# Kernel optimization log

Hardware: AMD Instinct MI355X
Metric: run time of the kernel (lower is better)

Reference implementation:

```python
import jax, jax.numpy as jnp
import numpy as np

IN_CH = 512
HEADS = 8
DIM_HEAD = 64
HIDDEN = HEADS * DIM_HEAD


def rms_norm(x, g):
    # torch F.normalize(x, dim=1): x / max(||x||_2 along channel, eps)
    norm = jnp.sqrt(jnp.sum(x * x, axis=1, keepdims=True))
    xn = x / jnp.maximum(norm, 1e-12)
    return xn * g * (x.shape[1] ** 0.5)


def setup_inputs() -> dict:
    key = jax.random.key(0)
    ks = jax.random.split(key, 6)
    x = jax.random.normal(ks[0], (8, IN_CH, 8192), dtype=jnp.float32)
    g1 = jnp.ones((1, IN_CH, 1), dtype=jnp.float32)
    # Conv1d k=1 weights stored as [out, in]
    w_qkv = jax.random.normal(ks[1], (3 * HIDDEN, IN_CH), dtype=jnp.float32) * (IN_CH ** -0.5)
    w_out = jax.random.normal(ks[2], (IN_CH, HIDDEN), dtype=jnp.float32) * (HIDDEN ** -0.5)
    b_out = jax.random.normal(ks[3], (IN_CH,), dtype=jnp.float32) * 0.01
    g2 = jnp.ones((1, IN_CH, 1), dtype=jnp.float32)
    return {"x": x, "g1": g1, "w_qkv": w_qkv, "w_out": w_out, "b_out": b_out, "g2": g2}


def reference(x, g1, w_qkv, w_out, b_out, g2):
    b, c, l = x.shape
    h, dh = HEADS, DIM_HEAD
    scale = dh ** -0.5
    xn = rms_norm(x, g1)
    # 1x1 conv == channel matmul: [b,3*hidden,l]
    qkv = jnp.einsum('oc,bcl->bol', w_qkv, xn)
    q, k, v = jnp.split(qkv, 3, axis=1)
    q = q.reshape(b, h, dh, l)
    k = k.reshape(b, h, dh, l)
    v = v.reshape(b, h, dh, l)
    q = jax.nn.softmax(q, axis=2) * scale  # softmax over head-dim channels
    k = jax.nn.softmax(k, axis=3)          # softmax over sequence
    context = jnp.einsum('bhdn,bhen->bhde', k, v)  # [b,h,dh,dh]
    out = jnp.einsum('bhde,bhdn->bhen', context, q)
    out = out.reshape(b, h * dh, l)
    out = jnp.einsum('oc,bcl->bol', w_out, out) + b_out[None, :, None]
    return rms_norm(out, g2)
```

## Files before the change

### kernel.cpp

```cpp
#include <hip/hip_runtime.h>
#include <hip/hip_bf16.h>


typedef short short8 __attribute__((ext_vector_type(8)));
typedef short short4v __attribute__((ext_vector_type(4)));
typedef float f32x4 __attribute__((ext_vector_type(4)));
typedef unsigned short ushort;

#define SQRT512 22.627416997969522f

__device__ __forceinline__ ushort f2bf(float f){
  union{float f; unsigned u;} v; v.f = f;
  unsigned r = v.u + 0x7fffu + ((v.u >> 16) & 1u);
  return (ushort)(r >> 16);
}

__device__ __forceinline__ void gload16(const void* g, void* l){
  __builtin_amdgcn_global_load_lds(
      (const __attribute__((address_space(1))) unsigned int*)(unsigned long long)g,
      (__attribute__((address_space(3))) unsigned int*)(unsigned int)(unsigned long long)l,
      16, 0, 0);
}

__global__ void k_prep_w1(const float* __restrict__ wqkv, const float* __restrict__ g1,
                          ushort* __restrict__ W1){
  int i = blockIdx.x * 256 + threadIdx.x;
  int c = i & 511;
  W1[i] = f2bf(wqkv[i] * g1[c] * SQRT512);
}

__global__ __launch_bounds__(256) void k_xt(const float* __restrict__ x,
                                            ushort* __restrict__ Xt,
                                            float* __restrict__ invnorm){
  __shared__ __align__(16) ushort tile[64*132];
  __shared__ float ssq[4][64];
  int b = blockIdx.y, lb = blockIdx.x;
  int t = threadIdx.x, lane = t & 63, crow = t >> 6;
  const float* xb = x + ((size_t)b*512)*8192 + (size_t)lb*64;
  float acc = 0.f;
  for(int c0 = 0; c0 < 512; c0 += 128){
    __syncthreads();
    for(int cc = crow; cc < 128; cc += 4){
      float v = xb[(size_t)(c0+cc)*8192 + lane];
      acc += v*v;
      tile[lane*132 + cc] = f2bf(v);
    }
    __syncthreads();
    ushort* dst = Xt + ((size_t)(b*8192 + lb*64))*512 + c0;
    int ch = t & 31;
    for(int r = t >> 5; r < 64; r += 8){
      short4v vv = *(const short4v*)&tile[r*132 + ch*4];
      *(short4v*)(dst + (size_t)r*512 + ch*4) = vv;
    }
  }
  ssq[crow][lane] = acc;
  __syncthreads();
  if(t < 64){
    float s = ssq[0][t] + ssq[1][t] + ssq[2][t] + ssq[3][t];
    invnorm[b*8192 + lb*64 + t] = 1.f / fmaxf(sqrtf(s), 1e-12f);
  }
}

__global__ __launch_bounds__(512,4) void k_qkv(
    const ushort* __restrict__ W1, const ushort* __restrict__ Xt,
    const float* __restrict__ invnorm,
    ushort* __restrict__ Qt, float* __restrict__ ctxp, float* __restrict__ kpart){
  __shared__ __align__(16) union U {
    ushort buf[2][12288];
    struct { ushort P[8192]; ushort Vb[8192]; } e;
  } S;
  __shared__ float ksum[128];

  int bid = blockIdx.x;
  int wg  = (bid & 7)*384 + (bid >> 3);
  int b   = wg / 384;
  int rem = wg % 384;
  int grp = rem / 12, s = rem % 12;
  bool isQ = (s < 4);
  int t = threadIdx.x, lane = t & 63, w = t >> 6;
  int rsub = lane >> 2;
  int pc   = (lane & 3) ^ ((lane >> 3) & 3);

  int r = 0, ct2 = 0, hb = 0, ct = 0;
  const ushort* Aq = W1;
  const ushort* Bbase;
  if(isQ){ r = s; ct2 = grp;
    Aq = W1 + (size_t)(r*128)*512;
    Bbase = Xt + ((size_t)(b*8192 + ct2*256))*512;
  } else { int t2 = s - 4; ct = 2*grp + (t2 & 1); hb = t2 >> 1;
    Bbase = Xt + ((size_t)(b*8192 + ct*128))*512;
  }
  if(t < 128) ksum[t] = 0.f;

  f32x4 acc[4][4] = {};

  auto stage = [&](int ks, int cb){
    int goff = ks*32 + pc*8;
    if(isQ){
      ushort* A  = S.buf[cb];
      ushort* Bl = S.buf[cb] + 4096;
      gload16(Aq    + (size_t)(w*16 + rsub)*512 + goff, A + w*512);
      gload16(Bbase + (size_t)(w*32 + rsub)*512 + goff, Bl + w*1024);
      gload16(Bbase + (size_t)(w*32 + 16 + rsub)*512 + goff, Bl + w*1024 + 512);
    } else {
      ushort* A  = S.buf[cb];
      ushort* Bl = S.buf[cb] + 8192;
      int lr0 = w*32 + rsub;
      int gr0 = (w < 4) ? (512 + hb*128 + lr0) : (1024 + hb*128 + (lr0 - 128));
      gload16(W1 + (size_t)gr0*512 + goff, A + w*1024);
      gload16(W1 + (size_t)(gr0 + 16)*512 + goff, A + w*1024 + 512);
      gload16(Bbase + (size_t)(w*16 + rsub)*512 + goff, Bl + w*512);
    }
  };

  auto compute = [&](int cb){
    const ushort *A, *Bl; int aw, bw;
    if(isQ){ A = S.buf[cb]; Bl = S.buf[cb] + 4096; aw = w >> 2; bw = w & 3; }
    else   { A = S.buf[cb]; Bl = S.buf[cb] + 8192; aw = w >> 1; bw = w & 1; }
    int g = lane >> 4;
    short8 af[4], bf[4];
#pragma unroll
    for(int m4 = 0; m4 < 4; ++m4){ int ra = aw*64 + m4*16 + (lane & 15);
      af[m4] = *(const short8*)&A[ra*32 + (g ^ ((ra >> 1) & 3))*8]; }
#pragma unroll
    for(int n4 = 0; n4 < 4; ++n4){ int rb = bw*64 + n4*16 + (lane & 15);
      bf[n4] = *(const short8*)&Bl[rb*32 + (g ^ ((rb >> 1) & 3))*8]; }
#pragma unroll
    for(int m4 = 0; m4 < 4; ++m4)
#pragma unroll
      for(int n4 = 0; n4 < 4; ++n4)
        acc[m4][n4] = __builtin_amdgcn_mfma_f32_16x16x32_bf16(af[m4], bf[n4], acc[m4][n4], 0,0,0);
  };

  stage(0, 0);
#pragma unroll
  for(int ks = 0; ks < 16; ++ks){
    int cur = ks & 1;
    if(ks < 15){ stage(ks + 1, cur ^ 1);
                 asm volatile("s_waitcnt vmcnt(3)" ::: "memory"); }
    else       { asm volatile("s_waitcnt vmcnt(0)" ::: "memory"); }
    __builtin_amdgcn_s_barrier();
    compute(cur);
    asm volatile("s_waitcnt lgkmcnt(0)" ::: "memory");
    __builtin_amdgcn_s_barrier();
  }

  if(isQ){
    int wr = w >> 2, wc = w & 3;
    float cs[4];
    const float* invb = invnorm + b*8192 + ct2*256;
#pragma unroll
    for(int n4 = 0; n4 < 4; ++n4) cs[n4] = invb[wc*64 + n4*16 + (lane & 15)];
    float mx[4] = {-3e38f,-3e38f,-3e38f,-3e38f};
#pragma unroll
    for(int m4 = 0; m4 < 4; ++m4)
#pragma unroll
      for(int n4 = 0; n4 < 4; ++n4)
#pragma unroll
        for(int j = 0; j < 4; ++j){
          float v = acc[m4][n4][j]*cs[n4];
          acc[m4][n4][j] = v;
          mx[n4] = fmaxf(mx[n4], v);
        }
#pragma unroll
    for(int n4 = 0; n4 < 4; ++n4){
      mx[n4] = fmaxf(mx[n4], __shfl_xor(mx[n4], 16));
      mx[n4] = fmaxf(mx[n4], __shfl_xor(mx[n4], 32));
    }
    float sm[4] = {0.f,0.f,0.f,0.f};
#pragma unroll
    for(int m4 = 0; m4 < 4; ++m4)
#pragma unroll
      for(int n4 = 0; n4 < 4; ++n4)
#pragma unroll
        for(int j = 0; j < 4; ++j){
          float e = __expf(acc[m4][n4][j] - mx[n4]);
          acc[m4][n4][j] = e;
          sm[n4] += e;
        }
    float inv[4];
#pragma unroll
    for(int n4 = 0; n4 < 4; ++n4){
      sm[n4] += __shfl_xor(sm[n4], 16);
      sm[n4] += __shfl_xor(sm[n4], 32);
      inv[n4] = 0.125f / sm[n4];
    }
#pragma unroll
    for(int n4 = 0; n4 < 4; ++n4){
      int col = ct2*256 + wc*64 + n4*16 + (lane & 15);
      ushort* dst = Qt + ((size_t)(b*8192 + col))*512 + r*128 + wr*64 + (lane >> 4)*4;
#pragma unroll
      for(int m4 = 0; m4 < 4; ++m4){
        short4v p;
#pragma unroll
        for(int j = 0; j < 4; ++j) p[j] = (short)f2bf(acc[m4][n4][j]*inv[n4]);
        *(short4v*)(dst + m4*16) = p;
      }
    }
  } else {
    int wr2 = w >> 1, bw = w & 1;
    bool isK = (w < 4);
    float cs[4];
    const float* invb = invnorm + b*8192 + ct*128;
#pragma unroll
    for(int n4 = 0; n4 < 4; ++n4) cs[n4] = invb[bw*64 + n4*16 + (lane & 15)];
    int hq = w >> 2, rq = w & 3;
    f32x4 c2[4] = {};
#pragma unroll
    for(int hl = 0; hl < 2; ++hl){
      __syncthreads();
      if(bw == hl){
#pragma unroll
        for(int m4 = 0; m4 < 4; ++m4)
#pragma unroll
          for(int j = 0; j < 4; ++j){
            int row = wr2*64 + m4*16 + (lane >> 4)*4 + j;
            float rs = 0.f;
#pragma unroll
            for(int n4 = 0; n4 < 4; ++n4){
              int lc = n4*16 + (lane & 15);
              float val = acc[m4][n4][j]*cs[n4];
              if(isK){
                float e = __expf(val); rs += e;
                S.e.P[row*64 + ((lc >> 3) ^ (row & 7))*8 + (lc & 7)] = f2bf(e);
              } else {
                int er = row - 128;
                S.e.Vb[er*64 + ((lc >> 3) ^ (er & 7))*8 + (lc & 7)] = f2bf(val);
              }
            }
            if(isK) atomicAdd(&ksum[row], rs);
          }
      }
      __syncthreads();
#pragma unroll
      for(int kk = 0; kk < 2; ++kk){
        int g2 = kk*4 + (lane >> 4);
        int da = hq*64 + rq*16 + (lane & 15);
        short8 pa = *(const short8*)&S.e.P[da*64 + (g2 ^ (da & 7))*8];
#pragma unroll
        for(int n4 = 0; n4 < 4; ++n4){
          int eb = hq*64 + n4*16 + (lane & 15);
          short8 vb = *(const short8*)&S.e.Vb[eb*64 + (g2 ^ (eb & 7))*8];
          c2[n4] = __builtin_amdgcn_mfma_f32_16x16x32_bf16(pa, vb, c2[n4], 0,0,0);
        }
      }
    }
    if(t < 128) kpart[(size_t)ct*4096 + b*512 + hb*128 + t] = ksum[t];
    float* dst = ctxp + ((size_t)((b*8 + hb*2 + hq)*64 + ct))*4096;
#pragma unroll
    for(int n4 = 0; n4 < 4; ++n4)
#pragma unroll
      for(int j = 0; j < 4; ++j){
        int d64 = rq*16 + (lane >> 4)*4 + j;
        int e   = n4*16 + (lane & 15);
        dst[d64*64 + e] = c2[n4][j];
      }
  }
}

__global__ void k_invz(const float* __restrict__ kpart, float* __restrict__ invZ){
  int row = blockIdx.x*256 + threadIdx.x;
  float s = 0.f;
  for(int c = 0; c < 64; ++c) s += kpart[(size_t)c*4096 + row];
  invZ[row] = 1.f / s;
}

__global__ void k_m2(const float* __restrict__ ctxp, const float* __restrict__ invZ,
                     const float* __restrict__ Wout, ushort* __restrict__ M2){
  __shared__ __align__(16) ushort ctxl[4096];
  int bh = blockIdx.x, b = bh >> 3, h = bh & 7;
  int t = threadIdx.x, lane = t & 63, w = t >> 6;
  for(int i = t; i < 4096; i += 512){
    float s = 0.f;
    for(int sp = 0; sp < 64; ++sp) s += ctxp[((size_t)(bh*64 + sp))*4096 + i];
    int d = i >> 6, e = i & 63;
    s *= invZ[bh*64 + d];
    ctxl[(e >> 3)*512 + d*8 + (e & 7)] = f2bf(s);
  }
  __syncthreads();
  f32x4 acc[4][4] = {};
#pragma unroll
  for(int kk = 0; kk < 2; ++kk){
    int g = kk*4 + (lane >> 4);
    short8 bf[4];
#pragma unroll
    for(int n4 = 0; n4 < 4; ++n4)
      bf[n4] = *(const short8*)&ctxl[g*512 + (n4*16 + (lane & 15))*8];
    int e0 = (lane >> 4)*8 + kk*32;
#pragma unroll
    for(int m4 = 0; m4 < 4; ++m4){
      int o = w*64 + m4*16 + (lane & 15);
      const float* wp = Wout + (size_t)o*512 + h*64 + e0;
      float4 w0 = *(const float4*)(wp);
      float4 w1 = *(const float4*)(wp + 4);
      short8 af;
      af[0]=(short)f2bf(w0.x); af[1]=(short)f2bf(w0.y); af[2]=(short)f2bf(w0.z); af[3]=(short)f2bf(w0.w);
      af[4]=(short)f2bf(w1.x); af[5]=(short)f2bf(w1.y); af[6]=(short)f2bf(w1.z); af[7]=(short)f2bf(w1.w);
#pragma unroll
      for(int n4 = 0; n4 < 4; ++n4)
        acc[m4][n4] = __builtin_amdgcn_mfma_f32_16x16x32_bf16(af, bf[n4], acc[m4][n4], 0,0,0);
    }
  }
  ushort* dst = M2 + (size_t)b*512*512 + h*64;
#pragma unroll
  for(int m4 = 0; m4 < 4; ++m4)
#pragma unroll
    for(int n4 = 0; n4 < 4; ++n4)
#pragma unroll
      for(int j = 0; j < 4; ++j){
        int o = w*64 + m4*16 + (lane >> 4)*4 + j;
        int d = n4*16 + (lane & 15);
        dst[(size_t)o*512 + d] = f2bf(acc[m4][n4][j]);
      }
}

__global__ __launch_bounds__(512,2) void k_out(const ushort* __restrict__ M2,
                                               const ushort* __restrict__ Qt,
                                               const float* __restrict__ bout,
                                               const float* __restrict__ g2,
                                               float* __restrict__ out){
  __shared__ __align__(16) ushort A[16384];
  __shared__ __align__(16) ushort Bs[2048];
  __shared__ float colss[64];
  __shared__ float bo[512], gg[512];
  int bid = blockIdx.x;
  int wg = (bid & 7)*128 + (bid >> 3);
  int b = wg >> 7, lb = wg & 127;
  int t = threadIdx.x, lane = t & 63, w = t >> 6;
  bo[t & 511] = bout[t & 511];
  gg[t & 511] = g2[t & 511];
  if(t < 64) colss[t] = 0.f;
  const ushort* Abase = M2 + (size_t)b*262144;
  const ushort* Bbase = Qt + ((size_t)(b*8192 + lb*64))*512;
  int rsub = lane >> 2;
  int pc   = (lane & 3) ^ ((lane >> 3) & 3);
  f32x4 acc[4][4] = {};
  for(int ks = 0; ks < 16; ++ks){
    int goff = ks*32 + pc*8;
#pragma unroll
    for(int j = 0; j < 4; ++j){
      int m = w*4 + j;
      gload16(Abase + (size_t)(m*16 + rsub)*512 + goff, &A[m*512]);
    }
    if(w >= 4){
      int m = w - 4;
      gload16(Bbase + (size_t)(m*16 + rsub)*512 + goff, &Bs[m*512]);
    }
    __syncthreads();
    int g = lane >> 4;
    short8 bf[4];
#pragma unroll
    for(int n4 = 0; n4 < 4; ++n4){
      int rb = n4*16 + (lane & 15);
      bf[n4] = *(const short8*)&Bs[rb*32 + (g ^ ((rb >> 1) & 3))*8];
    }
#pragma unroll
    for(int m4 = 0; m4 < 4; ++m4){
      int ra = w*64 + m4*16 + (lane & 15);
      short8 af = *(const short8*)&A[ra*32 + (g ^ ((ra >> 1) & 3))*8];
#pragma unroll
      for(int n4 = 0; n4 < 4; ++n4)
        acc[m4][n4] = __builtin_amdgcn_mfma_f32_16x16x32_bf16(af, bf[n4], acc[m4][n4], 0,0,0);
    }
    __syncthreads();
  }
  float ps[4] = {0.f,0.f,0.f,0.f};
#pragma unroll
  for(int m4 = 0; m4 < 4; ++m4)
#pragma unroll
    for(int j = 0; j < 4; ++j){
      int o = w*64 + m4*16 + (lane >> 4)*4 + j;
      float bb = bo[o];
#pragma unroll
      for(int n4 = 0; n4 < 4; ++n4){
        float v = acc[m4][n4][j] + bb;
        acc[m4][n4][j] = v;
        ps[n4] += v*v;
      }
    }
#pragma unroll
  for(int n4 = 0; n4 < 4; ++n4) atomicAdd(&colss[n4*16 + (lane & 15)], ps[n4]);
  __syncthreads();
  float csc[4];
#pragma unroll
  for(int n4 = 0; n4 < 4; ++n4)
    csc[n4] = SQRT512 / fmaxf(sqrtf(colss[n4*16 + (lane & 15)]), 1e-12f);
  float* obase = out + ((size_t)b*512)*8192 + lb*64;
#pragma unroll
  for(int m4 = 0; m4 < 4; ++m4)
#pragma unroll
    for(int j = 0; j < 4; ++j){
      int o = w*64 + m4*16 + (lane >> 4)*4 + j;
      float gv = gg[o];
#pragma unroll
      for(int n4 = 0; n4 < 4; ++n4)
        obase[(size_t)o*8192 + n4*16 + (lane & 15)] = acc[m4][n4][j]*csc[n4]*gv;
    }
}

extern "C" void kernel_launch(void* const* d_in, const int* in_sizes, int n_in,
                              void* d_out, int out_size, void* d_ws, size_t ws_size,
                              hipStream_t stream){
  const float* x    = (const float*)d_in[0];
  const float* g1   = (const float*)d_in[1];
  const float* wqkv = (const float*)d_in[2];
  const float* wout = (const float*)d_in[3];
  const float* bout = (const float*)d_in[4];
  const float* g2   = (const float*)d_in[5];
  float* out = (float*)d_out;
  char* ws = (char*)d_ws;
  const size_t MB = 1024*1024;
  ushort* Qt      = (ushort*)(ws);
  float*  ctxp    = (float*) (ws + 64*MB);
  ushort* W1      = (ushort*)(ws + 132*MB);
  float*  invnorm = (float*) (ws + 134*MB);
  float*  kpart   = (float*) (ws + 135*MB);
  float*  invZ    = (float*) (ws + 136*MB);
  ushort* M2      = (ushort*)(ws + 137*MB);
  ushort* Xt = (ushort*)d_out;

  k_prep_w1<<<3072, 256, 0, stream>>>(wqkv, g1, W1);
  k_xt<<<dim3(128, 8), 256, 0, stream>>>(x, Xt, invnorm);
  k_qkv<<<3072, 512, 0, stream>>>(W1, Xt, invnorm, Qt, ctxp, kpart);
  k_invz<<<16, 256, 0, stream>>>(kpart, invZ);
  k_m2<<<64, 512, 0, stream>>>(ctxp, invZ, wout, M2);
  k_out<<<1024, 512, 0, stream>>>(M2, Qt, bout, g2, out);
}
```

Before: 402.9 us.

## Split fused QKV kernel into K/V-context and Q kernels with sequence-looped partials

Splits the combined Q/KV kernel into two kernels. The K/V kernel loops over four 128-column sequence tiles per block and accumulates context in registers, cutting the context partials from 64 to 16 per head. That shrinks the ctxp write traffic and the reduction work in k_m2 and k_invz. The Q kernel stages its softmax output through LDS so Qt stores are coalesced, and the ksum atomics are first reduced with wave shuffles. The cost is fewer, longer K/V blocks, which lowers parallelism and adds an extra kernel launch.

```diff
diff --git a/kernel.cpp b/kernel.cpp
--- a/kernel.cpp
+++ b/kernel.cpp
@@ -61,151 +61,72 @@
   }
 }
 
-__global__ __launch_bounds__(512,4) void k_qkv(
+__global__ __launch_bounds__(512) void k_kvctx(
     const ushort* __restrict__ W1, const ushort* __restrict__ Xt,
     const float* __restrict__ invnorm,
-    ushort* __restrict__ Qt, float* __restrict__ ctxp, float* __restrict__ kpart){
-  __shared__ __align__(16) union U {
-    ushort buf[2][12288];
+    float* __restrict__ ctxp, float* __restrict__ kpart){
+  __shared__ __align__(16) union {
+    struct { ushort A[2][8192]; ushort B[2][4096]; } m;
     struct { ushort P[8192]; ushort Vb[8192]; } e;
   } S;
   __shared__ float ksum[128];
 
   int bid = blockIdx.x;
-  int wg  = (bid & 7)*384 + (bid >> 3);
-  int b   = wg / 384;
-  int rem = wg % 384;
-  int grp = rem / 12, s = rem % 12;
-  bool isQ = (s < 4);
+  int wg  = (bid & 7)*64 + (bid >> 3);
+  int b   = wg >> 6;
+  int rem = wg & 63;
+  int lt  = rem >> 2, hb = rem & 3;
   int t = threadIdx.x, lane = t & 63, w = t >> 6;
-  int rsub = lane >> 2;
-  int pc   = (lane & 3) ^ ((lane >> 3) & 3);
-
-  int r = 0, ct2 = 0, hb = 0, ct = 0;
-  const ushort* Aq = W1;
-  const ushort* Bbase;
-  if(isQ){ r = s; ct2 = grp;
-    Aq = W1 + (size_t)(r*128)*512;
-    Bbase = Xt + ((size_t)(b*8192 + ct2*256))*512;
-  } else { int t2 = s - 4; ct = 2*grp + (t2 & 1); hb = t2 >> 1;
-    Bbase = Xt + ((size_t)(b*8192 + ct*128))*512;
-  }
+  int aw = w >> 1, bw = w & 1;
+  int hq = w >> 2, rq = w & 3;
+  int pcs = (lane & 3) ^ ((lane >> 2) & 3);
+
   if(t < 128) ksum[t] = 0.f;
-
-  f32x4 acc[4][4] = {};
-
-  auto stage = [&](int ks, int cb){
-    int goff = ks*32 + pc*8;
-    if(isQ){
-      ushort* A  = S.buf[cb];
-      ushort* Bl = S.buf[cb] + 4096;
-      gload16(Aq    + (size_t)(w*16 + rsub)*512 + goff, A + w*512);
-      gload16(Bbase + (size_t)(w*32 + rsub)*512 + goff, Bl + w*1024);
-      gload16(Bbase + (size_t)(w*32 + 16 + rsub)*512 + goff, Bl + w*1024 + 512);
-    } else {
-      ushort* A  = S.buf[cb];
-      ushort* Bl = S.buf[cb] + 8192;
-      int lr0 = w*32 + rsub;
-      int gr0 = (w < 4) ? (512 + hb*128 + lr0) : (1024 + hb*128 + (lr0 - 128));
-      gload16(W1 + (size_t)gr0*512 + goff, A + w*1024);
-      gload16(W1 + (size_t)(gr0 + 16)*512 + goff, A + w*1024 + 512);
-      gload16(Bbase + (size_t)(w*16 + rsub)*512 + goff, Bl + w*512);
-    }
-  };
-
-  auto compute = [&](int cb){
-    const ushort *A, *Bl; int aw, bw;
-    if(isQ){ A = S.buf[cb]; Bl = S.buf[cb] + 4096; aw = w >> 2; bw = w & 3; }
-    else   { A = S.buf[cb]; Bl = S.buf[cb] + 8192; aw = w >> 1; bw = w & 1; }
-    int g = lane >> 4;
-    short8 af[4], bf[4];
-#pragma unroll
-    for(int m4 = 0; m4 < 4; ++m4){ int ra = aw*64 + m4*16 + (lane & 15);
-      af[m4] = *(const short8*)&A[ra*32 + (g ^ ((ra >> 1) & 3))*8]; }
-#pragma unroll
-    for(int n4 = 0; n4 < 4; ++n4){ int rb = bw*64 + n4*16 + (lane & 15);
-      bf[n4] = *(const short8*)&Bl[rb*32 + (g ^ ((rb >> 1) & 3))*8]; }
-#pragma unroll
-    for(int m4 = 0; m4 < 4; ++m4)
-#pragma unroll
-      for(int n4 = 0; n4 < 4; ++n4)
-        acc[m4][n4] = __builtin_amdgcn_mfma_f32_16x16x32_bf16(af[m4], bf[n4], acc[m4][n4], 0,0,0);
-  };
-
-  stage(0, 0);
-#pragma unroll
-  for(int ks = 0; ks < 16; ++ks){
-    int cur = ks & 1;
-    if(ks < 15){ stage(ks + 1, cur ^ 1);
-                 asm volatile("s_waitcnt vmcnt(3)" ::: "memory"); }
-    else       { asm volatile("s_waitcnt vmcnt(0)" ::: "memory"); }
-    __builtin_amdgcn_s_barrier();
-    compute(cur);
-    asm volatile("s_waitcnt lgkmcnt(0)" ::: "memory");
-    __builtin_amdgcn_s_barrier();
-  }
-
-  if(isQ){
-    int wr = w >> 2, wc = w & 3;
+  __syncthreads();
+
+  f32x4 c2[4] = {};
+
+  for(int s = 0; s < 4; ++s){
+    int l0 = lt*512 + s*128;
+    f32x4 acc[4][4] = {};
+
+    auto stage = [&](int kt, int cb){
+      int goff = kt*32 + pcs*8;
+      int r0 = w*16 + (lane >> 2);
+      gload16(W1 + (size_t)(512  + hb*128 + r0)*512 + goff, &S.m.A[cb][w*512]);
+      gload16(W1 + (size_t)(1024 + hb*128 + r0)*512 + goff, &S.m.A[cb][4096 + w*512]);
+      gload16(Xt + ((size_t)(b*8192 + l0 + r0))*512 + goff, &S.m.B[cb][w*512]);
+    };
+
+    stage(0, 0);
+    for(int kt = 0; kt < 16; ++kt){
+      int cur = kt & 1;
+      if(kt < 15){ stage(kt + 1, cur ^ 1);
+                   asm volatile("s_waitcnt vmcnt(3)" ::: "memory"); }
+      else       { asm volatile("s_waitcnt vmcnt(0)" ::: "memory"); }
+      __builtin_amdgcn_s_barrier();
+      int g = lane >> 4;
+      short8 af[4], bf[4];
+#pragma unroll
+      for(int m4 = 0; m4 < 4; ++m4){ int ra = aw*64 + m4*16 + (lane & 15);
+        af[m4] = *(const short8*)&S.m.A[cur][ra*32 + ((g ^ (ra & 3)))*8]; }
+#pragma unroll
+      for(int n4 = 0; n4 < 4; ++n4){ int rb = bw*64 + n4*16 + (lane & 15);
+        bf[n4] = *(const short8*)&S.m.B[cur][rb*32 + ((g ^ (rb & 3)))*8]; }
+#pragma unroll
+      for(int m4 = 0; m4 < 4; ++m4)
+#pragma unroll
+        for(int n4 = 0; n4 < 4; ++n4)
+          acc[m4][n4] = __builtin_amdgcn_mfma_f32_16x16x32_bf16(af[m4], bf[n4], acc[m4][n4], 0,0,0);
+      asm volatile("s_waitcnt lgkmcnt(0)" ::: "memory");
+      __builtin_amdgcn_s_barrier();
+    }
+
     float cs[4];
-    const float* invb = invnorm + b*8192 + ct2*256;
-#pragma unroll
-    for(int n4 = 0; n4 < 4; ++n4) cs[n4] = invb[wc*64 + n4*16 + (lane & 15)];
-    float mx[4] = {-3e38f,-3e38f,-3e38f,-3e38f};
-#pragma unroll
-    for(int m4 = 0; m4 < 4; ++m4)
-#pragma unroll
-      for(int n4 = 0; n4 < 4; ++n4)
-#pragma unroll
-        for(int j = 0; j < 4; ++j){
-          float v = acc[m4][n4][j]*cs[n4];
-          acc[m4][n4][j] = v;
-          mx[n4] = fmaxf(mx[n4], v);
-        }
-#pragma unroll
-    for(int n4 = 0; n4 < 4; ++n4){
-      mx[n4] = fmaxf(mx[n4], __shfl_xor(mx[n4], 16));
-      mx[n4] = fmaxf(mx[n4], __shfl_xor(mx[n4], 32));
-    }
-    float sm[4] = {0.f,0.f,0.f,0.f};
-#pragma unroll
-    for(int m4 = 0; m4 < 4; ++m4)
-#pragma unroll
-      for(int n4 = 0; n4 < 4; ++n4)
-#pragma unroll
-        for(int j = 0; j < 4; ++j){
-          float e = __expf(acc[m4][n4][j] - mx[n4]);
-          acc[m4][n4][j] = e;
-          sm[n4] += e;
-        }
-    float inv[4];
-#pragma unroll
-    for(int n4 = 0; n4 < 4; ++n4){
-      sm[n4] += __shfl_xor(sm[n4], 16);
-      sm[n4] += __shfl_xor(sm[n4], 32);
-      inv[n4] = 0.125f / sm[n4];
-    }
-#pragma unroll
-    for(int n4 = 0; n4 < 4; ++n4){
-      int col = ct2*256 + wc*64 + n4*16 + (lane & 15);
-      ushort* dst = Qt + ((size_t)(b*8192 + col))*512 + r*128 + wr*64 + (lane >> 4)*4;
-#pragma unroll
-      for(int m4 = 0; m4 < 4; ++m4){
-        short4v p;
-#pragma unroll
-        for(int j = 0; j < 4; ++j) p[j] = (short)f2bf(acc[m4][n4][j]*inv[n4]);
-        *(short4v*)(dst + m4*16) = p;
-      }
-    }
-  } else {
-    int wr2 = w >> 1, bw = w & 1;
+    const float* invb = invnorm + b*8192 + l0;
+#pragma unroll
+    for(int n4 = 0; n4 < 4; ++n4) cs[n4] = invb[bw*64 + n4*16 + (lane & 15)];
     bool isK = (w < 4);
-    float cs[4];
-    const float* invb = invnorm + b*8192 + ct*128;
-#pragma unroll
-    for(int n4 = 0; n4 < 4; ++n4) cs[n4] = invb[bw*64 + n4*16 + (lane & 15)];
-    int hq = w >> 2, rq = w & 3;
-    f32x4 c2[4] = {};
 #pragma unroll
     for(int hl = 0; hl < 2; ++hl){
       __syncthreads();
@@ -214,7 +135,7 @@
         for(int m4 = 0; m4 < 4; ++m4)
 #pragma unroll
           for(int j = 0; j < 4; ++j){
-            int row = wr2*64 + m4*16 + (lane >> 4)*4 + j;
+            int row = aw*64 + m4*16 + (lane >> 4)*4 + j;
             float rs = 0.f;
 #pragma unroll
             for(int n4 = 0; n4 < 4; ++n4){
@@ -228,7 +149,11 @@
                 S.e.Vb[er*64 + ((lc >> 3) ^ (er & 7))*8 + (lc & 7)] = f2bf(val);
               }
             }
-            if(isK) atomicAdd(&ksum[row], rs);
+            if(isK){
+              rs += __shfl_xor(rs, 1); rs += __shfl_xor(rs, 2);
+              rs += __shfl_xor(rs, 4); rs += __shfl_xor(rs, 8);
+              if((lane & 15) == 0) atomicAdd(&ksum[row], rs);
+            }
           }
       }
       __syncthreads();
@@ -245,23 +170,136 @@
         }
       }
     }
-    if(t < 128) kpart[(size_t)ct*4096 + b*512 + hb*128 + t] = ksum[t];
-    float* dst = ctxp + ((size_t)((b*8 + hb*2 + hq)*64 + ct))*4096;
+    __syncthreads();
+  }
+
+  float* dst = ctxp + ((size_t)((b*8 + hb*2 + hq)*16 + lt))*4096;
+#pragma unroll
+  for(int n4 = 0; n4 < 4; ++n4)
+#pragma unroll
+    for(int j = 0; j < 4; ++j){
+      int d = rq*16 + (lane >> 4)*4 + j, e = n4*16 + (lane & 15);
+      dst[d*64 + e] = c2[n4][j];
+    }
+  if(t < 128) kpart[(size_t)lt*4096 + b*512 + hb*128 + t] = ksum[t];
+}
+
+__global__ __launch_bounds__(512) void k_q(
+    const ushort* __restrict__ W1, const ushort* __restrict__ Xt,
+    const float* __restrict__ invnorm, ushort* __restrict__ Qt){
+  __shared__ __align__(16) union {
+    struct { ushort A[2][4096]; ushort B[2][8192]; } m;
+    ushort T[128*136];
+  } S;
+  int bid = blockIdx.x;
+  int wg  = (bid & 7)*128 + (bid >> 3);
+  int b   = wg >> 7;
+  int rem = wg & 127;
+  int nt  = rem >> 2, mt = rem & 3;
+  int t = threadIdx.x, lane = t & 63, w = t >> 6;
+  int aw = w >> 2, bw = w & 3;
+  int pcs = (lane & 3) ^ ((lane >> 2) & 3);
+
+  f32x4 acc[4][4] = {};
+
+  auto stage = [&](int kt, int cb){
+    int goff = kt*32 + pcs*8;
+    int r0 = w*16 + (lane >> 2);
+    gload16(W1 + (size_t)(mt*128 + r0)*512 + goff, &S.m.A[cb][w*512]);
+    gload16(Xt + ((size_t)(b*8192 + nt*256 + r0))*512 + goff, &S.m.B[cb][w*512]);
+    gload16(Xt + ((size_t)(b*8192 + nt*256 + 128 + r0))*512 + goff, &S.m.B[cb][4096 + w*512]);
+  };
+
+  stage(0, 0);
+  for(int kt = 0; kt < 16; ++kt){
+    int cur = kt & 1;
+    if(kt < 15){ stage(kt + 1, cur ^ 1);
+                 asm volatile("s_waitcnt vmcnt(3)" ::: "memory"); }
+    else       { asm volatile("s_waitcnt vmcnt(0)" ::: "memory"); }
+    __builtin_amdgcn_s_barrier();
+    int g = lane >> 4;
+    short8 af[4], bf[4];
+#pragma unroll
+    for(int m4 = 0; m4 < 4; ++m4){ int ra = aw*64 + m4*16 + (lane & 15);
+      af[m4] = *(const short8*)&S.m.A[cur][ra*32 + ((g ^ (ra & 3)))*8]; }
+#pragma unroll
+    for(int n4 = 0; n4 < 4; ++n4){ int rb = bw*64 + n4*16 + (lane & 15);
+      bf[n4] = *(const short8*)&S.m.B[cur][rb*32 + ((g ^ (rb & 3)))*8]; }
+#pragma unroll
+    for(int m4 = 0; m4 < 4; ++m4)
+#pragma unroll
+      for(int n4 = 0; n4 < 4; ++n4)
+        acc[m4][n4] = __builtin_amdgcn_mfma_f32_16x16x32_bf16(af[m4], bf[n4], acc[m4][n4], 0,0,0);
+    asm volatile("s_waitcnt lgkmcnt(0)" ::: "memory");
+    __builtin_amdgcn_s_barrier();
+  }
+
+  float cs[4];
+  const float* invb = invnorm + b*8192 + nt*256;
+#pragma unroll
+  for(int n4 = 0; n4 < 4; ++n4) cs[n4] = invb[bw*64 + n4*16 + (lane & 15)];
+  float mx[4] = {-3e38f,-3e38f,-3e38f,-3e38f};
+#pragma unroll
+  for(int m4 = 0; m4 < 4; ++m4)
 #pragma unroll
     for(int n4 = 0; n4 < 4; ++n4)
 #pragma unroll
       for(int j = 0; j < 4; ++j){
-        int d64 = rq*16 + (lane >> 4)*4 + j;
-        int e   = n4*16 + (lane & 15);
-        dst[d64*64 + e] = c2[n4][j];
-      }
+        float v = acc[m4][n4][j]*cs[n4];
+        acc[m4][n4][j] = v;
+        mx[n4] = fmaxf(mx[n4], v);
+      }
+#pragma unroll
+  for(int n4 = 0; n4 < 4; ++n4){
+    mx[n4] = fmaxf(mx[n4], __shfl_xor(mx[n4], 16));
+    mx[n4] = fmaxf(mx[n4], __shfl_xor(mx[n4], 32));
+  }
+  float sm[4] = {0.f,0.f,0.f,0.f};
+#pragma unroll
+  for(int m4 = 0; m4 < 4; ++m4)
+#pragma unroll
+    for(int n4 = 0; n4 < 4; ++n4)
+#pragma unroll
+      for(int j = 0; j < 4; ++j){
+        float e = __expf(acc[m4][n4][j] - mx[n4]);
+        acc[m4][n4][j] = e;
+        sm[n4] += e;
+      }
+  float inv[4];
+#pragma unroll
+  for(int n4 = 0; n4 < 4; ++n4){
+    sm[n4] += __shfl_xor(sm[n4], 16);
+    sm[n4] += __shfl_xor(sm[n4], 32);
+    inv[n4] = 0.125f / sm[n4];
+  }
+#pragma unroll
+  for(int p = 0; p < 2; ++p){
+    __syncthreads();
+    if((bw >> 1) == p){
+#pragma unroll
+      for(int m4 = 0; m4 < 4; ++m4)
+#pragma unroll
+        for(int n4 = 0; n4 < 4; ++n4)
+#pragma unroll
+          for(int j = 0; j < 4; ++j){
+            int lloc = (bw & 1)*64 + n4*16 + (lane & 15);
+            int hidl = aw*64 + m4*16 + (lane >> 4)*4 + j;
+            S.T[lloc*136 + hidl] = f2bf(acc[m4][n4][j]*inv[n4]);
+          }
+    }
+    __syncthreads();
+    int rr = t >> 2, cc = t & 3;
+    ushort* gdst = Qt + ((size_t)(b*8192 + nt*256 + p*128 + rr))*512 + mt*128 + cc*32;
+#pragma unroll
+    for(int u = 0; u < 4; ++u)
+      *(short8*)(gdst + u*8) = *(const short8*)&S.T[rr*136 + cc*32 + u*8];
   }
 }
 
 __global__ void k_invz(const float* __restrict__ kpart, float* __restrict__ invZ){
   int row = blockIdx.x*256 + threadIdx.x;
   float s = 0.f;
-  for(int c = 0; c < 64; ++c) s += kpart[(size_t)c*4096 + row];
+  for(int c = 0; c < 16; ++c) s += kpart[(size_t)c*4096 + row];
   invZ[row] = 1.f / s;
 }
 
@@ -272,7 +310,7 @@
   int t = threadIdx.x, lane = t & 63, w = t >> 6;
   for(int i = t; i < 4096; i += 512){
     float s = 0.f;
-    for(int sp = 0; sp < 64; ++sp) s += ctxp[((size_t)(bh*64 + sp))*4096 + i];
+    for(int sp = 0; sp < 16; ++sp) s += ctxp[((size_t)(bh*16 + sp))*4096 + i];
     int d = i >> 6, e = i & 63;
     s *= invZ[bh*64 + d];
     ctxl[(e >> 3)*512 + d*8 + (e & 7)] = f2bf(s);
@@ -411,17 +449,18 @@
   char* ws = (char*)d_ws;
   const size_t MB = 1024*1024;
   ushort* Qt      = (ushort*)(ws);
-  float*  ctxp    = (float*) (ws + 64*MB);
-  ushort* W1      = (ushort*)(ws + 132*MB);
-  float*  invnorm = (float*) (ws + 134*MB);
-  float*  kpart   = (float*) (ws + 135*MB);
-  float*  invZ    = (float*) (ws + 136*MB);
-  ushort* M2      = (ushort*)(ws + 137*MB);
+  ushort* W1      = (ushort*)(ws + 64*MB);
+  float*  invnorm = (float*) (ws + 66*MB);
+  float*  kpart   = (float*) (ws + 67*MB);
+  float*  invZ    = (float*) (ws + 68*MB);
+  float*  ctxp    = (float*) (ws + 69*MB);
+  ushort* M2      = (ushort*)(ws + 85*MB);
   ushort* Xt = (ushort*)d_out;
 
   k_prep_w1<<<3072, 256, 0, stream>>>(wqkv, g1, W1);
   k_xt<<<dim3(128, 8), 256, 0, stream>>>(x, Xt, invnorm);
-  k_qkv<<<3072, 512, 0, stream>>>(W1, Xt, invnorm, Qt, ctxp, kpart);
+  k_kvctx<<<512, 512, 0, stream>>>(W1, Xt, invnorm, ctxp, kpart);
+  k_q<<<1024, 512, 0, stream>>>(W1, Xt, invnorm, Qt);
   k_invz<<<16, 256, 0, stream>>>(kpart, invZ);
   k_m2<<<64, 512, 0, stream>>>(ctxp, invZ, wout, M2);
   k_out<<<1024, 512, 0, stream>>>(M2, Qt, bout, g2, out);
```

Result: slower. 462.4 us (+14.8%).
